# Kernel tuning notes

Hardware: AMD Instinct MI355X
Metric: run time of the kernel (lower is better)

## Reference

```python
import jax, jax.numpy as jnp
import numpy as np

B, L, D_MODEL = 16, 512, 768
S, D_LLM = 2048, 4096
H = 8
E = D_MODEL // H  # d_keys = 96


def setup_inputs() -> dict:
    key = jax.random.key(0)
    ks = jax.random.split(key, 10)
    sc_dm = 1.0 / np.sqrt(D_MODEL)
    sc_dl = 1.0 / np.sqrt(D_LLM)
    return {
        "target": jax.random.normal(ks[0], (B, L, D_MODEL), jnp.float32),
        "source": jax.random.normal(ks[1], (S, D_LLM), jnp.float32),
        "Wq": jax.random.normal(ks[2], (D_MODEL, H * E), jnp.float32) * sc_dm,
        "bq": jnp.zeros((H * E,), jnp.float32),
        "Wk": jax.random.normal(ks[3], (D_LLM, H * E), jnp.float32) * sc_dl,
        "bk": jnp.zeros((H * E,), jnp.float32),
        "Wv": jax.random.normal(ks[4], (D_LLM, H * E), jnp.float32) * sc_dl,
        "bv": jnp.zeros((H * E,), jnp.float32),
        "Wo": jax.random.normal(ks[5], (H * E, D_LLM), jnp.float32) * sc_dm,
        "bo": jnp.zeros((D_LLM,), jnp.float32),
    }


def reference(target, source, Wq, bq, Wk, bk, Wv, bv, Wo, bo):
    # Q: (B, L, H, E); K, V: (S, H, E) -- K/V are shared across the batch.
    Q = (target @ Wq + bq).reshape(B, L, H, E)
    K = (source @ Wk + bk).reshape(S, H, E)
    V = (source @ Wv + bv).reshape(S, H, E)
    # scores: (B, H, L, S)
    scores = jnp.einsum('blhe,she->bhls', Q, K) / jnp.sqrt(jnp.asarray(E, Q.dtype))
    attn = jax.nn.softmax(scores, axis=-1)  # dropout is identity in eval mode
    rep = jnp.einsum('bhls,she->blhe', attn, V).reshape(B, L, H * E)
    return rep @ Wo + bo  # (B, L, d_llm)
```

## Files before the change

### kernel.cpp

```cpp
#include <hip/hip_runtime.h>
#include <hip/hip_bf16.h>
#include <stdint.h>

typedef __hip_bfloat16 bf16;
typedef __attribute__((ext_vector_type(8))) short short8;
typedef __attribute__((ext_vector_type(4))) float floatx4;

__device__ __forceinline__ void gll16(const bf16* g, const bf16* lds_base) {
  __builtin_amdgcn_global_load_lds(
      (const __attribute__((address_space(1))) unsigned int*)g,
      (__attribute__((address_space(3))) unsigned int*)lds_base,
      16, 0, 0);
}

__global__ __launch_bounds__(256) void cvt_both(const float* __restrict__ t_in,
                                                const float* __restrict__ s_in,
                                                bf16* __restrict__ t_out,
                                                bf16* __restrict__ s_out) {
  int bid = blockIdx.x;
  const float* in;
  bf16* out;
  int i;
  if (bid < 6144) {
    in = t_in; out = t_out; i = (bid * 256 + threadIdx.x) * 4;
  } else {
    in = s_in; out = s_out; i = ((bid - 6144) * 256 + threadIdx.x) * 4;
  }
  float4 v = *(const float4*)(in + i);
  out[i + 0] = __float2bfloat16(v.x);
  out[i + 1] = __float2bfloat16(v.y);
  out[i + 2] = __float2bfloat16(v.z);
  out[i + 3] = __float2bfloat16(v.w);
}

__global__ __launch_bounds__(256) void trans_all(const float* __restrict__ Wq,
                                                 const float* __restrict__ Wk,
                                                 const float* __restrict__ Wv,
                                                 const float* __restrict__ Wo,
                                                 bf16* __restrict__ WqT,
                                                 bf16* __restrict__ WkvT,
                                                 bf16* __restrict__ WoT) {
  __shared__ float t[32][33];
  int id = blockIdx.x;
  const float* in; bf16* out; int R, C, cx, ry;
  if (id < 576)        { in = Wq; out = WqT; R = 768;  C = 768;  id -= 0;    cx = id % 24;  ry = id / 24; }
  else if (id < 3648)  { in = Wk; out = WkvT; R = 4096; C = 768; id -= 576;  cx = id % 24;  ry = id / 24; }
  else if (id < 6720)  { in = Wv; out = WkvT + (size_t)768 * 4096; R = 4096; C = 768; id -= 3648; cx = id % 24; ry = id / 24; }
  else                 { in = Wo; out = WoT; R = 768;  C = 4096; id -= 6720; cx = id % 128; ry = id / 128; }
  int tx = threadIdx.x & 31, ty = threadIdx.x >> 5;
  int c0 = cx * 32, r0 = ry * 32;
#pragma unroll
  for (int j = 0; j < 4; ++j)
    t[ty + j * 8][tx] = in[(size_t)(r0 + ty + j * 8) * C + c0 + tx];
  __syncthreads();
#pragma unroll
  for (int j = 0; j < 4; ++j)
    out[(size_t)(c0 + ty + j * 8) * R + r0 + tx] = __float2bfloat16(t[tx][ty + j * 8]);
}

template <bool OUT_F32>
__global__ __launch_bounds__(256) void gemm_bt(const bf16* __restrict__ A,
                                               const bf16* __restrict__ BT,
                                               const float* __restrict__ bias,
                                               void* __restrict__ Cv,
                                               int M, int N, int K, int ldc) {
  __shared__ bf16 As[128 * 32];
  __shared__ bf16 Bs[128 * 32];
  const int tid = threadIdx.x;
  const int w = tid >> 6, lane = tid & 63;
  const int ln = lane & 15, quad = lane >> 4;
  const int wm = w >> 1, wn = w & 1;
  const int m0 = blockIdx.x * 128, n0 = blockIdx.y * 128;

  floatx4 acc[4][4] = {};

  for (int k0 = 0; k0 < K; k0 += 32) {
    __syncthreads();
#pragma unroll
    for (int t = 0; t < 2; ++t) {
      int cidb = (w * 2 + t) * 64;
      int cid = cidb + lane;
      int row = cid >> 2, ko = (cid & 3) * 8;
      gll16(A + (size_t)(m0 + row) * K + k0 + ko, As + cidb * 8);
      gll16(BT + (size_t)(n0 + row) * K + k0 + ko, Bs + cidb * 8);
    }
    __syncthreads();
    const short8* Av = (const short8*)As;
    const short8* Bv = (const short8*)Bs;
    short8 a[4], b[4];
#pragma unroll
    for (int mt = 0; mt < 4; ++mt) a[mt] = Av[(wm * 64 + mt * 16 + ln) * 4 + quad];
#pragma unroll
    for (int nt = 0; nt < 4; ++nt) b[nt] = Bv[(wn * 64 + nt * 16 + ln) * 4 + quad];
#pragma unroll
    for (int mt = 0; mt < 4; ++mt)
#pragma unroll
      for (int nt = 0; nt < 4; ++nt)
        acc[mt][nt] = __builtin_amdgcn_mfma_f32_16x16x32_bf16(a[mt], b[nt], acc[mt][nt], 0, 0, 0);
  }

#pragma unroll
  for (int nt = 0; nt < 4; ++nt) {
    int n = n0 + wn * 64 + nt * 16 + ln;
    float bv_ = bias[n];
#pragma unroll
    for (int mt = 0; mt < 4; ++mt)
#pragma unroll
      for (int r = 0; r < 4; ++r) {
        int m = m0 + wm * 64 + mt * 16 + quad * 4 + r;
        float v = acc[mt][nt][r] + bv_;
        size_t idx = (size_t)m * ldc + n;
        if (OUT_F32)
          ((float*)Cv)[idx] = v;
        else
          ((bf16*)Cv)[idx] = __float2bfloat16(v);
      }
  }
}

__global__ __launch_bounds__(256) void gemm_kv_splitk(const bf16* __restrict__ A,
                                                      const bf16* __restrict__ BT,
                                                      float* __restrict__ P) {
  __shared__ bf16 As[128 * 32];
  __shared__ bf16 Bs[128 * 32];
  const int tid = threadIdx.x;
  const int w = tid >> 6, lane = tid & 63;
  const int ln = lane & 15, quad = lane >> 4;
  const int wm = w >> 1, wn = w & 1;
  const int m0 = blockIdx.x * 128, n0 = blockIdx.y * 128;
  const int kbeg = blockIdx.z * 2048;
  float* Pz = P + (size_t)blockIdx.z * 2048 * 1536;

  floatx4 acc[4][4] = {};

  for (int k0 = kbeg; k0 < kbeg + 2048; k0 += 32) {
    __syncthreads();
#pragma unroll
    for (int t = 0; t < 2; ++t) {
      int cidb = (w * 2 + t) * 64;
      int cid = cidb + lane;
      int row = cid >> 2, ko = (cid & 3) * 8;
      gll16(A + (size_t)(m0 + row) * 4096 + k0 + ko, As + cidb * 8);
      gll16(BT + (size_t)(n0 + row) * 4096 + k0 + ko, Bs + cidb * 8);
    }
    __syncthreads();
    const short8* Av = (const short8*)As;
    const short8* Bv = (const short8*)Bs;
    short8 a[4], b[4];
#pragma unroll
    for (int mt = 0; mt < 4; ++mt) a[mt] = Av[(wm * 64 + mt * 16 + ln) * 4 + quad];
#pragma unroll
    for (int nt = 0; nt < 4; ++nt) b[nt] = Bv[(wn * 64 + nt * 16 + ln) * 4 + quad];
#pragma unroll
    for (int mt = 0; mt < 4; ++mt)
#pragma unroll
      for (int nt = 0; nt < 4; ++nt)
        acc[mt][nt] = __builtin_amdgcn_mfma_f32_16x16x32_bf16(a[mt], b[nt], acc[mt][nt], 0, 0, 0);
  }

#pragma unroll
  for (int nt = 0; nt < 4; ++nt) {
    int n = n0 + wn * 64 + nt * 16 + ln;
#pragma unroll
    for (int mt = 0; mt < 4; ++mt)
#pragma unroll
      for (int r = 0; r < 4; ++r) {
        int m = m0 + wm * 64 + mt * 16 + quad * 4 + r;
        Pz[(size_t)m * 1536 + n] = acc[mt][nt][r];
      }
  }
}

__global__ __launch_bounds__(256) void reduce_kv_both(const float* __restrict__ P,
                                                      const float* __restrict__ bk,
                                                      const float* __restrict__ bv,
                                                      bf16* __restrict__ Kws,
                                                      bf16* __restrict__ VTws) {
  __shared__ float t[32][33];
  const float* p1 = P + (size_t)2048 * 1536;
  if (blockIdx.y == 0) {
    int idx = (blockIdx.x * 256 + threadIdx.x) * 4;
    int m = idx / 768, n = idx % 768;
    const float* q0 = P + (size_t)m * 1536 + n;
    const float* q1 = p1 + (size_t)m * 1536 + n;
    float4 a = *(const float4*)q0, b = *(const float4*)q1;
    float4 bb = *(const float4*)(bk + n);
    Kws[(size_t)m * 768 + n + 0] = __float2bfloat16(a.x + b.x + bb.x);
    Kws[(size_t)m * 768 + n + 1] = __float2bfloat16(a.y + b.y + bb.y);
    Kws[(size_t)m * 768 + n + 2] = __float2bfloat16(a.z + b.z + bb.z);
    Kws[(size_t)m * 768 + n + 3] = __float2bfloat16(a.w + b.w + bb.w);
  } else {
    int tx = threadIdx.x & 31, ty = threadIdx.x >> 5;
    int c0 = (blockIdx.x % 24) * 32;
    int r0 = (blockIdx.x / 24) * 32;
#pragma unroll
    for (int j = 0; j < 4; ++j) {
      size_t off = (size_t)(r0 + ty + j * 8) * 1536 + 768 + c0 + tx;
      t[ty + j * 8][tx] = P[off] + p1[off];
    }
    __syncthreads();
#pragma unroll
    for (int j = 0; j < 4; ++j) {
      int e = c0 + ty + j * 8;
      VTws[(size_t)e * 2048 + r0 + tx] = __float2bfloat16(t[tx][ty + j * 8] + bv[e]);
    }
  }
}

__global__ __launch_bounds__(256, 3) void attn_kernel(const bf16* __restrict__ Q,
                                                      const bf16* __restrict__ Kt,
                                                      const bf16* __restrict__ VT,
                                                      bf16* __restrict__ rep) {
  __shared__ bf16 Ks[2][64 * 13 * 8];
  __shared__ bf16 Ps[128 * 72];

  const int tid = threadIdx.x, w = tid >> 6, lane = tid & 63;
  const int ln = lane & 15, quad = lane >> 4;
  const int qt = blockIdx.x;
  const int bh = blockIdx.y;
  const int b = bh >> 3, h = bh & 7;

  const bf16* Qg = Q + (size_t)(b * 512 + qt * 128) * 768 + h * 96;
  short8 qf[2][3];
#pragma unroll
  for (int mt = 0; mt < 2; ++mt)
#pragma unroll
    for (int es = 0; es < 3; ++es)
      qf[mt][es] = *(const short8*)(Qg + (size_t)(w * 32 + mt * 16 + ln) * 768 + (es * 4 + quad) * 8);

  const bf16* Kgh = Kt + h * 96;
  const bf16* Vgh = VT + (size_t)h * 96 * 2048;

  int krow[3], koff[3];
#pragma unroll
  for (int t = 0; t < 3; ++t) {
    int cid = t * 256 + tid;
    krow[t] = cid / 12;
    koff[t] = cid % 12;
  }

  short8 kreg[3];
#pragma unroll
  for (int t = 0; t < 3; ++t)
    kreg[t] = *(const short8*)(Kgh + (size_t)krow[t] * 768 + koff[t] * 8);
#pragma unroll
  for (int t = 0; t < 3; ++t)
    *(short8*)(&Ks[0][(krow[t] * 13 + koff[t]) * 8]) = kreg[t];

  floatx4 po[2][6] = {};
  float psum[8] = {};
  const float cexp = 1.4426950408889634f / 9.797958971132712f;

  for (int it = 0; it < 32; ++it) {
    const int s0 = it * 64;
    __syncthreads();

    if (it < 31) {
#pragma unroll
      for (int t = 0; t < 3; ++t)
        kreg[t] = *(const short8*)(Kgh + (size_t)(s0 + 64 + krow[t]) * 768 + koff[t] * 8);
    }

    floatx4 sacc[2][4] = {};
    const short8* Kv = (const short8*)Ks[it & 1];
#pragma unroll
    for (int es = 0; es < 3; ++es) {
      short8 bb[4];
#pragma unroll
      for (int ct = 0; ct < 4; ++ct) bb[ct] = Kv[(ct * 16 + ln) * 13 + es * 4 + quad];
#pragma unroll
      for (int mt = 0; mt < 2; ++mt)
#pragma unroll
        for (int ct = 0; ct < 4; ++ct)
          sacc[mt][ct] = __builtin_amdgcn_mfma_f32_16x16x32_bf16(qf[mt][es], bb[ct], sacc[mt][ct], 0, 0, 0);
    }

#pragma unroll
    for (int mt = 0; mt < 2; ++mt)
#pragma unroll
      for (int ct = 0; ct < 4; ++ct)
#pragma unroll
        for (int r = 0; r < 4; ++r) {
          float p = exp2f(sacc[mt][ct][r] * cexp);
          psum[mt * 4 + r] += p;
          Ps[(w * 32 + mt * 16 + quad * 4 + r) * 72 + ct * 16 + ln] = __float2bfloat16(p);
        }

    const short8* Pv = (const short8*)Ps;
#pragma unroll
    for (int ks = 0; ks < 2; ++ks) {
      short8 a[2];
#pragma unroll
      for (int mt = 0; mt < 2; ++mt) a[mt] = Pv[(w * 32 + mt * 16 + ln) * 9 + ks * 4 + quad];
#pragma unroll
      for (int nt = 0; nt < 6; ++nt) {
        short8 bb = *(const short8*)(Vgh + (size_t)(nt * 16 + ln) * 2048 + s0 + (ks * 4 + quad) * 8);
#pragma unroll
        for (int mt = 0; mt < 2; ++mt)
          po[mt][nt] = __builtin_amdgcn_mfma_f32_16x16x32_bf16(a[mt], bb, po[mt][nt], 0, 0, 0);
      }
    }

    if (it < 31) {
      bf16* dst = Ks[(it + 1) & 1];
#pragma unroll
      for (int t = 0; t < 3; ++t)
        *(short8*)(&dst[(krow[t] * 13 + koff[t]) * 8]) = kreg[t];
    }
  }

  float linv[8];
#pragma unroll
  for (int i = 0; i < 8; ++i) {
    float v = psum[i];
    v += __shfl_xor(v, 1, 64);
    v += __shfl_xor(v, 2, 64);
    v += __shfl_xor(v, 4, 64);
    v += __shfl_xor(v, 8, 64);
    linv[i] = 1.f / fmaxf(v, 1e-37f);
  }

  bf16* og = rep + (size_t)(b * 512 + qt * 128) * 768 + h * 96;
#pragma unroll
  for (int mt = 0; mt < 2; ++mt)
#pragma unroll
    for (int nt = 0; nt < 6; ++nt)
#pragma unroll
      for (int r = 0; r < 4; ++r) {
        int row = w * 32 + mt * 16 + quad * 4 + r;
        int e = nt * 16 + ln;
        og[(size_t)row * 768 + e] = __float2bfloat16(po[mt][nt][r] * linv[mt * 4 + r]);
      }
}

extern "C" void kernel_launch(void* const* d_in, const int* in_sizes, int n_in,
                              void* d_out, int out_size, void* d_ws, size_t ws_size,
                              hipStream_t stream) {
  const float* target = (const float*)d_in[0];
  const float* source = (const float*)d_in[1];
  const float* Wq = (const float*)d_in[2];
  const float* bq = (const float*)d_in[3];
  const float* Wk = (const float*)d_in[4];
  const float* bk = (const float*)d_in[5];
  const float* Wv = (const float*)d_in[6];
  const float* bv = (const float*)d_in[7];
  const float* Wo = (const float*)d_in[8];
  const float* bo = (const float*)d_in[9];
  float* out = (float*)d_out;

  bf16* ws = (bf16*)d_ws;
  bf16* tgt_bf = ws;
  bf16* src_bf = tgt_bf + 6291456;
  bf16* WqT = src_bf + 8388608;
  bf16* WkvT = WqT + 589824;
  bf16* WoT = WkvT + 6291456;
  bf16* Qws = WoT + 3145728;
  bf16* Kws = Qws + 6291456;
  bf16* VTws = Kws + 1572864;
  float* Pkv = (float*)(ws + 34144256);
  const size_t NEED_SPLIT = 68288512ull + 25165824ull;
  bf16* repws = src_bf;

  cvt_both<<<14336, 256, 0, stream>>>(target, source, tgt_bf, src_bf);
  trans_all<<<9792, 256, 0, stream>>>(Wq, Wk, Wv, Wo, WqT, WkvT, WoT);

  gemm_bt<false><<<dim3(64, 6), 256, 0, stream>>>(tgt_bf, WqT, bq, Qws, 8192, 768, 768, 768);

  if (ws_size >= NEED_SPLIT) {
    gemm_kv_splitk<<<dim3(16, 12, 2), 256, 0, stream>>>(src_bf, WkvT, Pkv);
    reduce_kv_both<<<dim3(1536, 2), 256, 0, stream>>>(Pkv, bk, bv, Kws, VTws);
  } else {
    gemm_bt<false><<<dim3(16, 6), 256, 0, stream>>>(src_bf, WkvT, bk, Kws, 2048, 768, 4096, 768);
    gemm_bt<false><<<dim3(16, 6), 256, 0, stream>>>(src_bf, WkvT + (size_t)768 * 4096, bv, Kws, 2048, 768, 4096, 768);
  }

  attn_kernel<<<dim3(4, 128), 256, 0, stream>>>(Qws, Kws, VTws, repws);

  gemm_bt<true><<<dim3(64, 32), 256, 0, stream>>>(repws, WoT, bo, out, 8192, 4096, 768, 4096);
}
```

Baseline: 525.5 us.

## Halve attention query tile and stage V tiles through LDS

The attention kernel now processes 64 query rows per block instead of 128, launching twice as many blocks, and raises the occupancy hint from 3 to 4 blocks per CU. V tiles are now prefetched into registers and stored in a padded LDS buffer alongside K, replacing per-wave direct global loads of V in the PV matmul. K is single-buffered with an extra barrier per iteration. The change aims to improve occupancy and memory coalescing for V, at the cost of less reuse of K/V per block, double the K/V global traffic overall, and an extra sync per step.

New measurement: 481.7 us. 8.3% less time.

```diff
diff --git a/kernel.cpp b/kernel.cpp
--- a/kernel.cpp
+++ b/kernel.cpp
@@ -207,12 +207,13 @@
   }
 }
 
-__global__ __launch_bounds__(256, 3) void attn_kernel(const bf16* __restrict__ Q,
+__global__ __launch_bounds__(256, 4) void attn_kernel(const bf16* __restrict__ Q,
                                                       const bf16* __restrict__ Kt,
                                                       const bf16* __restrict__ VT,
                                                       bf16* __restrict__ rep) {
-  __shared__ bf16 Ks[2][64 * 13 * 8];
-  __shared__ bf16 Ps[128 * 72];
+  __shared__ bf16 Ks[64 * 13 * 8];
+  __shared__ bf16 Vs[96 * 9 * 8];
+  __shared__ bf16 Ps[64 * 72];
 
   const int tid = threadIdx.x, w = tid >> 6, lane = tid & 63;
   const int ln = lane & 15, quad = lane >> 4;
@@ -220,98 +221,89 @@
   const int bh = blockIdx.y;
   const int b = bh >> 3, h = bh & 7;
 
-  const bf16* Qg = Q + (size_t)(b * 512 + qt * 128) * 768 + h * 96;
-  short8 qf[2][3];
-#pragma unroll
-  for (int mt = 0; mt < 2; ++mt)
-#pragma unroll
-    for (int es = 0; es < 3; ++es)
-      qf[mt][es] = *(const short8*)(Qg + (size_t)(w * 32 + mt * 16 + ln) * 768 + (es * 4 + quad) * 8);
+  const bf16* Qg = Q + (size_t)(b * 512 + qt * 64) * 768 + h * 96;
+  short8 qf[3];
+#pragma unroll
+  for (int es = 0; es < 3; ++es)
+    qf[es] = *(const short8*)(Qg + (size_t)(w * 16 + ln) * 768 + (es * 4 + quad) * 8);
 
   const bf16* Kgh = Kt + h * 96;
   const bf16* Vgh = VT + (size_t)h * 96 * 2048;
 
-  int krow[3], koff[3];
+  int krow[3], koff[3], vrow[3], voff[3];
 #pragma unroll
   for (int t = 0; t < 3; ++t) {
     int cid = t * 256 + tid;
-    krow[t] = cid / 12;
-    koff[t] = cid % 12;
-  }
-
-  short8 kreg[3];
-#pragma unroll
-  for (int t = 0; t < 3; ++t)
+    krow[t] = cid / 12; koff[t] = cid % 12;
+    vrow[t] = cid >> 3; voff[t] = cid & 7;
+  }
+
+  short8 kreg[3], vreg[3];
+#pragma unroll
+  for (int t = 0; t < 3; ++t) {
     kreg[t] = *(const short8*)(Kgh + (size_t)krow[t] * 768 + koff[t] * 8);
-#pragma unroll
-  for (int t = 0; t < 3; ++t)
-    *(short8*)(&Ks[0][(krow[t] * 13 + koff[t]) * 8]) = kreg[t];
-
-  floatx4 po[2][6] = {};
-  float psum[8] = {};
+    vreg[t] = *(const short8*)(Vgh + (size_t)vrow[t] * 2048 + voff[t] * 8);
+  }
+
+  floatx4 po[6] = {};
+  float psum[4] = {};
   const float cexp = 1.4426950408889634f / 9.797958971132712f;
 
   for (int it = 0; it < 32; ++it) {
     const int s0 = it * 64;
     __syncthreads();
 
+#pragma unroll
+    for (int t = 0; t < 3; ++t) {
+      *(short8*)(&Ks[(krow[t] * 13 + koff[t]) * 8]) = kreg[t];
+      *(short8*)(&Vs[(vrow[t] * 9 + voff[t]) * 8]) = vreg[t];
+    }
     if (it < 31) {
 #pragma unroll
-      for (int t = 0; t < 3; ++t)
+      for (int t = 0; t < 3; ++t) {
         kreg[t] = *(const short8*)(Kgh + (size_t)(s0 + 64 + krow[t]) * 768 + koff[t] * 8);
-    }
-
-    floatx4 sacc[2][4] = {};
-    const short8* Kv = (const short8*)Ks[it & 1];
+        vreg[t] = *(const short8*)(Vgh + (size_t)vrow[t] * 2048 + s0 + 64 + voff[t] * 8);
+      }
+    }
+    __syncthreads();
+
+    floatx4 sacc[4] = {};
+    const short8* Kv = (const short8*)Ks;
 #pragma unroll
     for (int es = 0; es < 3; ++es) {
       short8 bb[4];
 #pragma unroll
       for (int ct = 0; ct < 4; ++ct) bb[ct] = Kv[(ct * 16 + ln) * 13 + es * 4 + quad];
 #pragma unroll
-      for (int mt = 0; mt < 2; ++mt)
-#pragma unroll
-        for (int ct = 0; ct < 4; ++ct)
-          sacc[mt][ct] = __builtin_amdgcn_mfma_f32_16x16x32_bf16(qf[mt][es], bb[ct], sacc[mt][ct], 0, 0, 0);
-    }
-
-#pragma unroll
-    for (int mt = 0; mt < 2; ++mt)
-#pragma unroll
       for (int ct = 0; ct < 4; ++ct)
-#pragma unroll
-        for (int r = 0; r < 4; ++r) {
-          float p = exp2f(sacc[mt][ct][r] * cexp);
-          psum[mt * 4 + r] += p;
-          Ps[(w * 32 + mt * 16 + quad * 4 + r) * 72 + ct * 16 + ln] = __float2bfloat16(p);
-        }
+        sacc[ct] = __builtin_amdgcn_mfma_f32_16x16x32_bf16(qf[es], bb[ct], sacc[ct], 0, 0, 0);
+    }
+
+#pragma unroll
+    for (int ct = 0; ct < 4; ++ct)
+#pragma unroll
+      for (int r = 0; r < 4; ++r) {
+        float p = exp2f(sacc[ct][r] * cexp);
+        psum[r] += p;
+        Ps[(w * 16 + quad * 4 + r) * 72 + ct * 16 + ln] = __float2bfloat16(p);
+      }
 
     const short8* Pv = (const short8*)Ps;
+    const short8* Vv = (const short8*)Vs;
 #pragma unroll
     for (int ks = 0; ks < 2; ++ks) {
-      short8 a[2];
-#pragma unroll
-      for (int mt = 0; mt < 2; ++mt) a[mt] = Pv[(w * 32 + mt * 16 + ln) * 9 + ks * 4 + quad];
+      short8 a = Pv[(w * 16 + ln) * 9 + ks * 4 + quad];
 #pragma unroll
       for (int nt = 0; nt < 6; ++nt) {
-        short8 bb = *(const short8*)(Vgh + (size_t)(nt * 16 + ln) * 2048 + s0 + (ks * 4 + quad) * 8);
-#pragma unroll
-        for (int mt = 0; mt < 2; ++mt)
-          po[mt][nt] = __builtin_amdgcn_mfma_f32_16x16x32_bf16(a[mt], bb, po[mt][nt], 0, 0, 0);
-      }
-    }
-
-    if (it < 31) {
-      bf16* dst = Ks[(it + 1) & 1];
-#pragma unroll
-      for (int t = 0; t < 3; ++t)
-        *(short8*)(&dst[(krow[t] * 13 + koff[t]) * 8]) = kreg[t];
-    }
-  }
-
-  float linv[8];
-#pragma unroll
-  for (int i = 0; i < 8; ++i) {
+        short8 bb = Vv[(nt * 16 + ln) * 9 + ks * 4 + quad];
+        po[nt] = __builtin_amdgcn_mfma_f32_16x16x32_bf16(a, bb, po[nt], 0, 0, 0);
+      }
+    }
+  }
+
+  float linv[4];
+#pragma unroll
+  for (int i = 0; i < 4; ++i) {
     float v = psum[i];
     v += __shfl_xor(v, 1, 64);
     v += __shfl_xor(v, 2, 64);
@@ -320,17 +312,15 @@
     linv[i] = 1.f / fmaxf(v, 1e-37f);
   }
 
-  bf16* og = rep + (size_t)(b * 512 + qt * 128) * 768 + h * 96;
-#pragma unroll
-  for (int mt = 0; mt < 2; ++mt)
-#pragma unroll
-    for (int nt = 0; nt < 6; ++nt)
-#pragma unroll
-      for (int r = 0; r < 4; ++r) {
-        int row = w * 32 + mt * 16 + quad * 4 + r;
-        int e = nt * 16 + ln;
-        og[(size_t)row * 768 + e] = __float2bfloat16(po[mt][nt][r] * linv[mt * 4 + r]);
-      }
+  bf16* og = rep + (size_t)(b * 512 + qt * 64) * 768 + h * 96;
+#pragma unroll
+  for (int nt = 0; nt < 6; ++nt)
+#pragma unroll
+    for (int r = 0; r < 4; ++r) {
+      int row = w * 16 + quad * 4 + r;
+      int e = nt * 16 + ln;
+      og[(size_t)row * 768 + e] = __float2bfloat16(po[nt][r] * linv[r]);
+    }
 }
 
 extern "C" void kernel_launch(void* const* d_in, const int* in_sizes, int n_in,
@@ -374,7 +364,7 @@
     gemm_bt<false><<<dim3(16, 6), 256, 0, stream>>>(src_bf, WkvT + (size_t)768 * 4096, bv, Kws, 2048, 768, 4096, 768);
   }
 
-  attn_kernel<<<dim3(4, 128), 256, 0, stream>>>(Qws, Kws, VTws, repws);
+  attn_kernel<<<dim3(8, 128), 256, 0, stream>>>(Qws, Kws, VTws, repws);
 
   gemm_bt<true><<<dim3(64, 32), 256, 0, stream>>>(repws, WoT, bo, out, 8192, 4096, 768, 4096);
 }
```
